# Optimization experiments

Measured on AMD Instinct MI355X. Metric: run time of the kernel, lower is better.

Reference implementation:

```python
import jax, jax.numpy as jnp
import numpy as np

N_EMBD = 1024
N_HEADS = 16
HEAD_DIM = N_EMBD // N_HEADS


def setup_inputs() -> dict:
    key = jax.random.key(0)
    ks = jax.random.split(key, 12)
    B, T, S, C = 2, 2048, 2048, N_EMBD
    std = 1.0 / np.sqrt(C)
    inp = {
        "x": jax.random.normal(ks[0], (B, T, C), dtype=jnp.float32),
        "context": jax.random.normal(ks[1], (B, S, C), dtype=jnp.float32),
        "q_w": jax.random.uniform(ks[2], (C, C), minval=-std, maxval=std, dtype=jnp.float32),
        "q_b": jax.random.uniform(ks[3], (C,), minval=-std, maxval=std, dtype=jnp.float32),
        "k_w": jax.random.uniform(ks[4], (C, C), minval=-std, maxval=std, dtype=jnp.float32),
        "k_b": jax.random.uniform(ks[5], (C,), minval=-std, maxval=std, dtype=jnp.float32),
        "v_w": jax.random.uniform(ks[6], (C, C), minval=-std, maxval=std, dtype=jnp.float32),
        "v_b": jax.random.uniform(ks[7], (C,), minval=-std, maxval=std, dtype=jnp.float32),
        "o_w": jax.random.uniform(ks[8], (C, C), minval=-std, maxval=std, dtype=jnp.float32),
        "o_b": jax.random.uniform(ks[9], (C,), minval=-std, maxval=std, dtype=jnp.float32),
    }
    return inp


def reference(x, context, q_w, q_b, k_w, k_b, v_w, v_b, o_w, o_b):
    B, T, C = x.shape
    S = context.shape[1]
    H, D = N_HEADS, HEAD_DIM
    # projections (torch Linear: y = x @ W^T + b; here weights stored as [in, out])
    q = (x @ q_w + q_b).reshape(B, T, H, D).transpose(0, 2, 1, 3)        # [B,H,T,D]
    k = (context @ k_w + k_b).reshape(B, S, H, D).transpose(0, 2, 1, 3)  # [B,H,S,D]
    v = (context @ v_w + v_b).reshape(B, S, H, D).transpose(0, 2, 1, 3)  # [B,H,S,D]
    att = jnp.einsum("bhtd,bhsd->bhts", q, k) / jnp.sqrt(jnp.float32(D))  # [B,H,T,S]
    causal = jnp.tril(jnp.ones((T, S), dtype=bool))                       # mask from tril buffer
    att = jnp.where(causal[None, None, :, :], att, -jnp.inf)
    att = jax.nn.softmax(att, axis=-1)
    y = jnp.einsum("bhts,bhsd->bhtd", att, v)                             # [B,H,T,D]
    y = y.transpose(0, 2, 1, 3).reshape(B, T, C)
    return y @ o_w + o_b
```

## Files before the change

kernel.cpp:

```cpp
#include <hip/hip_runtime.h>
#include <hip/hip_bf16.h>

using bf16 = __bf16;
using bf16x4 = __attribute__((ext_vector_type(4))) __bf16;
using bf16x8 = __attribute__((ext_vector_type(8))) __bf16;
using f32x4 = __attribute__((ext_vector_type(4))) float;
using u32 = unsigned int;

#define EXP2F(x) __builtin_amdgcn_exp2f(x)

__device__ __forceinline__ void gload16(const void* g, void* l) {
  __builtin_amdgcn_global_load_lds((const __attribute__((address_space(1))) u32*)g,
                                   (__attribute__((address_space(3))) u32*)l, 16, 0, 0);
}

__global__ __launch_bounds__(256) void cvt_kernel(const float4* __restrict__ a,
                                                  const float4* __restrict__ b,
                                                  bf16x4* __restrict__ out) {
  int g = blockIdx.x * blockDim.x + threadIdx.x;
  float4 v = (g < 1048576) ? a[g] : b[g - 1048576];
  bf16x4 o = {(bf16)v.x, (bf16)v.y, (bf16)v.z, (bf16)v.w};
  out[g] = o;
}

__global__ __launch_bounds__(256) void transpose_kernel(const float* __restrict__ w0,
                                                        const float* __restrict__ w1,
                                                        const float* __restrict__ w2,
                                                        const float* __restrict__ w3,
                                                        bf16* __restrict__ wtbase) {
  __shared__ float tile[32][33];
  const int z = blockIdx.z;
  const float* w = (z == 0) ? w0 : (z == 1) ? w1 : (z == 2) ? w2 : w3;
  bf16* wt = wtbase + (size_t)z * 1048576;
  int k0 = blockIdx.y * 32, n0 = blockIdx.x * 32;
  int tx = threadIdx.x, ty = threadIdx.y;
#pragma unroll
  for (int i = 0; i < 4; i++)
    tile[ty + i * 8][tx] = w[(size_t)(k0 + ty + i * 8) * 1024 + n0 + tx];
  __syncthreads();
#pragma unroll
  for (int i = 0; i < 4; i++)
    wt[(size_t)(n0 + ty + i * 8) * 1024 + k0 + tx] = (bf16)tile[tx][ty + i * 8];
}

template <int MODE>
__device__ __forceinline__ void gemm_body(char* __restrict__ smem,
                                          const bf16* __restrict__ A,
                                          const bf16* __restrict__ Bt,
                                          const float* __restrict__ bias,
                                          void* __restrict__ outp, int bx, int by,
                                          float oscale) {
  constexpr int K = 1024;
  bf16(*Cs)[136] = (bf16(*)[136])smem;

  const int tid = threadIdx.x;
  const int lane = tid & 63;
  const int w = tid >> 6;
  const int wr = w >> 1, wc = w & 1;
  const int m0 = by * 128, n0 = bx * 128;
  const int fr = lane & 15, lg = lane >> 4;

  const int p = lane & 3;
  const int r0 = w * 16 + (lane >> 2);
  const int r1 = r0 + 64;
  const char* gA0 = (const char*)(A + (size_t)(m0 + r0) * K) + ((p ^ ((r0 >> 1) & 3)) << 4);
  const char* gA1 = (const char*)(A + (size_t)(m0 + r1) * K) + ((p ^ ((r1 >> 1) & 3)) << 4);
  const char* gB0 = (const char*)(Bt + (size_t)(n0 + r0) * K) + ((p ^ ((r0 >> 1) & 3)) << 4);
  const char* gB1 = (const char*)(Bt + (size_t)(n0 + r1) * K) + ((p ^ ((r1 >> 1) & 3)) << 4);

  const int sA = (fr >> 1) & 3;
  int aoff[4], boff[4];
#pragma unroll
  for (int mi = 0; mi < 4; mi++)
    aoff[mi] = (wr * 64 + mi * 16 + fr) * 64 + ((lg ^ sA) << 4);
#pragma unroll
  for (int ni = 0; ni < 4; ni++)
    boff[ni] = 8192 + (wc * 64 + ni * 16 + fr) * 64 + ((lg ^ sA) << 4);

  f32x4 acc[4][4] = {};

  gload16(gA0, smem + w * 1024);
  gload16(gA1, smem + 4096 + w * 1024);
  gload16(gB0, smem + 8192 + w * 1024);
  gload16(gB1, smem + 12288 + w * 1024);

  int cur = 0;
  for (int k0 = 0; k0 < K; k0 += 32) {
    __syncthreads();
    if (k0 + 32 < K) {
      const int nb = (cur ^ 1) * 16384;
      const int go = (k0 + 32) * 2;
      gload16(gA0 + go, smem + nb + w * 1024);
      gload16(gA1 + go, smem + nb + 4096 + w * 1024);
      gload16(gB0 + go, smem + nb + 8192 + w * 1024);
      gload16(gB1 + go, smem + nb + 12288 + w * 1024);
    }
    const char* base = smem + cur * 16384;
    bf16x8 af[4], bfr[4];
#pragma unroll
    for (int mi = 0; mi < 4; mi++) af[mi] = *(const bf16x8*)(base + aoff[mi]);
#pragma unroll
    for (int ni = 0; ni < 4; ni++) bfr[ni] = *(const bf16x8*)(base + boff[ni]);
#pragma unroll
    for (int mi = 0; mi < 4; mi++)
#pragma unroll
      for (int ni = 0; ni < 4; ni++)
        acc[mi][ni] =
            __builtin_amdgcn_mfma_f32_16x16x32_bf16(af[mi], bfr[ni], acc[mi][ni], 0, 0, 0);
    cur ^= 1;
  }

  float bv[4];
#pragma unroll
  for (int ni = 0; ni < 4; ni++) bv[ni] = bias[n0 + wc * 64 + ni * 16 + fr];
#pragma unroll
  for (int mi = 0; mi < 4; mi++)
#pragma unroll
    for (int ni = 0; ni < 4; ni++)
#pragma unroll
      for (int j = 0; j < 4; j++) acc[mi][ni][j] = (acc[mi][ni][j] + bv[ni]) * oscale;

  if (MODE == 2) {
    float* O = (float*)outp;
#pragma unroll
    for (int mi = 0; mi < 4; mi++)
#pragma unroll
      for (int ni = 0; ni < 4; ni++)
#pragma unroll
        for (int j = 0; j < 4; j++) {
          int row = m0 + wr * 64 + mi * 16 + (lane >> 4) * 4 + j;
          int col = n0 + wc * 64 + ni * 16 + fr;
          O[(size_t)row * 1024 + col] = acc[mi][ni][j];
        }
    return;
  }

  __syncthreads();
#pragma unroll
  for (int mi = 0; mi < 4; mi++) {
    int r = wr * 64 + mi * 16 + (lane >> 4) * 4;
#pragma unroll
    for (int ni = 0; ni < 4; ni++) {
      int c = wc * 64 + ni * 16 + fr;
#pragma unroll
      for (int j = 0; j < 4; j++) Cs[r + j][c] = (bf16)acc[mi][ni][j];
    }
  }
  __syncthreads();

  bf16* O = (bf16*)outp;
  if (MODE == 0) {
    int row = tid >> 1, ch = (tid & 1) * 64;
    int rg = m0 + row;
    int b = rg >> 11, t_ = rg & 2047;
    int c0 = n0 + ch;
    int h = c0 >> 6;
    bf16* dst = O + ((size_t)(b * 16 + h) * 2048 + t_) * 64;
#pragma unroll
    for (int i = 0; i < 8; i++) *(bf16x8*)&dst[i * 8] = *(const bf16x8*)&Cs[row][ch + i * 8];
  } else {
    int colL = tid >> 1, sh = (tid & 1) * 64;
    int cg = n0 + colL;
    int h = cg >> 6, d = cg & 63;
    int rg = m0 + sh;
    int b = rg >> 11, s_ = rg & 2047;
    bf16* dst = O + ((size_t)((b * 16 + h) * 64 + d)) * 2048 + s_;
#pragma unroll
    for (int i = 0; i < 8; i++) {
      bf16x8 v;
#pragma unroll
      for (int jj = 0; jj < 8; jj++) v[jj] = Cs[sh + i * 8 + jj][colL];
      *(bf16x8*)&dst[i * 8] = v;
    }
  }
}

__global__ __launch_bounds__(256) void gemm_qkv_kernel(const bf16* __restrict__ xb,
                                                       const bf16* __restrict__ cb,
                                                       const bf16* __restrict__ wtbase,
                                                       const float* __restrict__ bq,
                                                       const float* __restrict__ bk,
                                                       const float* __restrict__ bv,
                                                       bf16* __restrict__ outbase) {
  __shared__ __align__(16) char smem[34816];
  const int lin = blockIdx.x;
  const int xcd = lin & 7, idx = lin >> 3;
  const int seq = xcd * 96 + idx;
  const int z = seq >> 8;
  const int rem = seq & 255;
  const int by = rem >> 3, bx = rem & 7;
  const bf16* A = (z == 0) ? xb : cb;
  const bf16* Wt = wtbase + (size_t)z * 1048576;
  const float* bias = (z == 0) ? bq : (z == 1) ? bk : bv;
  bf16* out = outbase + (size_t)z * 4194304;
  const float oscale = (z == 0) ? 0.125f * 1.4426950408889634f : 1.0f;
  if (z == 2)
    gemm_body<1>(smem, A, Wt, bias, (void*)out, bx, by, oscale);
  else
    gemm_body<0>(smem, A, Wt, bias, (void*)out, bx, by, oscale);
}

__global__ __launch_bounds__(256) void gemm_o_kernel(const bf16* __restrict__ A,
                                                     const bf16* __restrict__ Wt,
                                                     const float* __restrict__ bias,
                                                     float* __restrict__ out) {
  __shared__ __align__(16) char smem[34816];
  const int lin = blockIdx.x;
  const int xcd = lin & 7, idx = lin >> 3;
  const int seq = xcd * 32 + idx;
  const int by = seq >> 3, bx = seq & 7;
  gemm_body<2>(smem, A, Wt, bias, (void*)out, bx, by, 1.0f);
}

__global__ __launch_bounds__(256) void attn_kernel(const bf16* __restrict__ Q,
                                                   const bf16* __restrict__ Kc,
                                                   const bf16* __restrict__ Vt,
                                                   bf16* __restrict__ Y) {
  const int bh = blockIdx.x;
  const int qt = 31 - blockIdx.y;
  const int tid = threadIdx.x, lane = tid & 63, w = tid >> 6;
  const int lr = lane & 15, lg = lane >> 4;
  const int q0 = qt * 64 + w * 16;

  __shared__ __align__(16) bf16 Ks[64 * 64];
  __shared__ __align__(16) bf16 Vs[64 * 64];
  __shared__ __align__(16) bf16 Plds[4][16][72];

  const bf16* qb = Q + ((size_t)bh * 2048 + q0 + lr) * 64 + lg * 8;
  const bf16x8 qfB0 = *(const bf16x8*)qb;
  const bf16x8 qfB1 = *(const bf16x8*)(qb + 32);

  const bf16* Kbase = Kc + (size_t)bh * 2048 * 64;
  const bf16* Vbase = Vt + (size_t)bh * 64 * 2048;

  const int srow = tid >> 2;
  const int scol = (tid & 3) * 16;
  const int r7x = (srow & 7) * 8;
  const int d0 = srow * 64 + (scol ^ r7x);
  const int d1 = srow * 64 + ((scol + 8) ^ r7x);

  bf16x8 kr0, kr1, vr0, vr1;
  {
    const bf16* kp = Kbase + (size_t)srow * 64 + scol;
    kr0 = *(const bf16x8*)kp;
    kr1 = *(const bf16x8*)(kp + 8);
    const bf16* vp = Vbase + (size_t)srow * 2048 + scol;
    vr0 = *(const bf16x8*)vp;
    vr1 = *(const bf16x8*)(vp + 8);
  }

  f32x4 yacc[4] = {};
  float mrow = -__builtin_inff(), lrow = 0.0f;
  const int kxor = (lr & 7) * 8;

  for (int c = 0; c <= qt; ++c) {
    const int sbase = c * 64;
    __syncthreads();
    *(bf16x8*)&Ks[d0] = kr0;
    *(bf16x8*)&Ks[d1] = kr1;
    *(bf16x8*)&Vs[d0] = vr0;
    *(bf16x8*)&Vs[d1] = vr1;
    __syncthreads();

    {
      const int cn = (c < qt) ? c + 1 : c;
      const int sb = cn * 64;
      const bf16* kp = Kbase + (size_t)(sb + srow) * 64 + scol;
      kr0 = *(const bf16x8*)kp;
      kr1 = *(const bf16x8*)(kp + 8);
      const bf16* vp = Vbase + (size_t)srow * 2048 + sb + scol;
      vr0 = *(const bf16x8*)vp;
      vr1 = *(const bf16x8*)(vp + 8);
    }

    f32x4 st[4];
    __builtin_amdgcn_s_setprio(1);
#pragma unroll
    for (int h = 0; h < 4; ++h) {
      const int rb = (16 * h + lr) * 64;
      const bf16x8 kf0 = *(const bf16x8*)&Ks[rb + ((lg * 8) ^ kxor)];
      const bf16x8 kf1 = *(const bf16x8*)&Ks[rb + ((32 + lg * 8) ^ kxor)];
      f32x4 z = {};
      z = __builtin_amdgcn_mfma_f32_16x16x32_bf16(kf0, qfB0, z, 0, 0, 0);
      z = __builtin_amdgcn_mfma_f32_16x16x32_bf16(kf1, qfB1, z, 0, 0, 0);
      st[h] = z;
    }
    __builtin_amdgcn_s_setprio(0);
    if (c == qt) {
      const int qg = q0 + lr;
#pragma unroll
      for (int h = 0; h < 4; ++h)
#pragma unroll
        for (int j = 0; j < 4; ++j) {
          int sg = sbase + 16 * h + lg * 4 + j;
          if (sg > qg) st[h][j] = -__builtin_inff();
        }
    }
    float vmax = fmaxf(fmaxf(st[0][0], st[0][1]), fmaxf(st[0][2], st[0][3]));
#pragma unroll
    for (int h = 1; h < 4; ++h)
      vmax = fmaxf(vmax, fmaxf(fmaxf(st[h][0], st[h][1]), fmaxf(st[h][2], st[h][3])));
    vmax = fmaxf(vmax, __shfl_xor(vmax, 16));
    vmax = fmaxf(vmax, __shfl_xor(vmax, 32));

    if (!__all(vmax <= mrow)) {
      const float mnew = fmaxf(mrow, vmax);
      const float cf = EXP2F(mrow - mnew);
      mrow = mnew;
      lrow *= cf;
      float cfj[4];
#pragma unroll
      for (int j = 0; j < 4; ++j) cfj[j] = __shfl(cf, lg * 4 + j);
#pragma unroll
      for (int nf = 0; nf < 4; ++nf)
#pragma unroll
        for (int j = 0; j < 4; ++j) yacc[nf][j] *= cfj[j];
    }

    float rs = 0.0f;
#pragma unroll
    for (int h = 0; h < 4; ++h) {
      float p0 = EXP2F(st[h][0] - mrow);
      float p1 = EXP2F(st[h][1] - mrow);
      float p2 = EXP2F(st[h][2] - mrow);
      float p3 = EXP2F(st[h][3] - mrow);
      rs += (p0 + p1) + (p2 + p3);
      bf16x4 pk = {(bf16)p0, (bf16)p1, (bf16)p2, (bf16)p3};
      *(bf16x4*)&Plds[w][lr][16 * h + lg * 4] = pk;
    }
    rs += __shfl_xor(rs, 16);
    rs += __shfl_xor(rs, 32);
    lrow += rs;

    const bf16x8 pa0 = *(const bf16x8*)&Plds[w][lr][lg * 8];
    const bf16x8 pa1 = *(const bf16x8*)&Plds[w][lr][32 + lg * 8];
    __builtin_amdgcn_s_setprio(1);
#pragma unroll
    for (int nf = 0; nf < 4; ++nf) {
      const int rb = (nf * 16 + lr) * 64;
      const bf16x8 vf0 = *(const bf16x8*)&Vs[rb + ((lg * 8) ^ kxor)];
      const bf16x8 vf1 = *(const bf16x8*)&Vs[rb + ((32 + lg * 8) ^ kxor)];
      yacc[nf] = __builtin_amdgcn_mfma_f32_16x16x32_bf16(pa0, vf0, yacc[nf], 0, 0, 0);
      yacc[nf] = __builtin_amdgcn_mfma_f32_16x16x32_bf16(pa1, vf1, yacc[nf], 0, 0, 0);
    }
    __builtin_amdgcn_s_setprio(0);
  }

  const float rinv = 1.0f / lrow;
  float linv[4];
#pragma unroll
  for (int j = 0; j < 4; ++j) linv[j] = __shfl(rinv, lg * 4 + j);
  const int b = bh >> 4, h = bh & 15;
#pragma unroll
  for (int nf = 0; nf < 4; ++nf)
#pragma unroll
    for (int j = 0; j < 4; ++j) {
      int qg = q0 + lg * 4 + j;
      Y[((size_t)b * 2048 + qg) * 1024 + h * 64 + nf * 16 + lr] = (bf16)(yacc[nf][j] * linv[j]);
    }
}

extern "C" void kernel_launch(void* const* d_in, const int* in_sizes, int n_in,
                              void* d_out, int out_size, void* d_ws, size_t ws_size,
                              hipStream_t stream) {
  const float* x = (const float*)d_in[0];
  const float* ctx = (const float*)d_in[1];
  const float* q_w = (const float*)d_in[2];
  const float* q_b = (const float*)d_in[3];
  const float* k_w = (const float*)d_in[4];
  const float* k_b = (const float*)d_in[5];
  const float* v_w = (const float*)d_in[6];
  const float* v_b = (const float*)d_in[7];
  const float* o_w = (const float*)d_in[8];
  const float* o_b = (const float*)d_in[9];

  char* ws = (char*)d_ws;
  const size_t MB = 1024 * 1024;
  bf16* xb = (bf16*)(ws + 0);
  bf16* qwt = (bf16*)(ws + 16 * MB);
  bf16* Qws = (bf16*)(ws + 24 * MB);
  bf16* Kws = (bf16*)(ws + 32 * MB);
  bf16* Vt = (bf16*)(ws + 40 * MB);
  bf16* Yws = (bf16*)(ws + 48 * MB);
  bf16* owt = qwt + 3 * 1048576;
  bf16* cb = xb + 4194304;

  cvt_kernel<<<8192, 256, 0, stream>>>((const float4*)x, (const float4*)ctx, (bf16x4*)xb);

  dim3 tb(32, 8), tg(32, 32, 4);
  transpose_kernel<<<tg, tb, 0, stream>>>(q_w, k_w, v_w, o_w, qwt);

  gemm_qkv_kernel<<<768, 256, 0, stream>>>(xb, cb, qwt, q_b, k_b, v_b, Qws);

  attn_kernel<<<dim3(32, 32), 256, 0, stream>>>(Qws, Kws, Vt, Yws);

  gemm_o_kernel<<<256, 256, 0, stream>>>(Yws, owt, o_b, (float*)d_out);
}
```

Measured before the change: 117.8 us.

## Double attention query tile per wave and merge convert and transpose kernels

The attention kernel now gives each wave 32 query rows (two 16-row MFMA fragments) instead of 16, so every block covers 128 queries and each K/V chunk staged in LDS is reused across twice as many rows. The launch grid halves, and waves whose rows lie entirely before a chunk skip its compute to respect causality. Separately, the input bf16 conversion and the weight transpose are combined into one launch to save a kernel launch. In exchange, register pressure roughly doubles for the accumulators and softmax state, and causal load imbalance between waves in a block increases.

```diff
diff --git a/kernel.cpp b/kernel.cpp
--- a/kernel.cpp
+++ b/kernel.cpp
@@ -14,33 +14,37 @@
                                    (__attribute__((address_space(3))) u32*)l, 16, 0, 0);
 }
 
-__global__ __launch_bounds__(256) void cvt_kernel(const float4* __restrict__ a,
-                                                  const float4* __restrict__ b,
-                                                  bf16x4* __restrict__ out) {
-  int g = blockIdx.x * blockDim.x + threadIdx.x;
-  float4 v = (g < 1048576) ? a[g] : b[g - 1048576];
-  bf16x4 o = {(bf16)v.x, (bf16)v.y, (bf16)v.z, (bf16)v.w};
-  out[g] = o;
-}
-
-__global__ __launch_bounds__(256) void transpose_kernel(const float* __restrict__ w0,
-                                                        const float* __restrict__ w1,
-                                                        const float* __restrict__ w2,
-                                                        const float* __restrict__ w3,
-                                                        bf16* __restrict__ wtbase) {
+__global__ __launch_bounds__(256) void prep_kernel(const float4* __restrict__ x4,
+                                                   const float4* __restrict__ c4,
+                                                   bf16x4* __restrict__ xb4,
+                                                   const float* __restrict__ w0,
+                                                   const float* __restrict__ w1,
+                                                   const float* __restrict__ w2,
+                                                   const float* __restrict__ w3,
+                                                   bf16* __restrict__ wtbase) {
   __shared__ float tile[32][33];
-  const int z = blockIdx.z;
-  const float* w = (z == 0) ? w0 : (z == 1) ? w1 : (z == 2) ? w2 : w3;
-  bf16* wt = wtbase + (size_t)z * 1048576;
-  int k0 = blockIdx.y * 32, n0 = blockIdx.x * 32;
-  int tx = threadIdx.x, ty = threadIdx.y;
-#pragma unroll
-  for (int i = 0; i < 4; i++)
-    tile[ty + i * 8][tx] = w[(size_t)(k0 + ty + i * 8) * 1024 + n0 + tx];
-  __syncthreads();
-#pragma unroll
-  for (int i = 0; i < 4; i++)
-    wt[(size_t)(n0 + ty + i * 8) * 1024 + k0 + tx] = (bf16)tile[tx][ty + i * 8];
+  const int bid = blockIdx.x;
+  const int tid = threadIdx.x;
+  if (bid < 8192) {
+    int g = bid * 256 + tid;
+    float4 v = (g < 1048576) ? x4[g] : c4[g - 1048576];
+    bf16x4 o = {(bf16)v.x, (bf16)v.y, (bf16)v.z, (bf16)v.w};
+    xb4[g] = o;
+  } else {
+    const int t = bid - 8192;
+    const int z = t >> 10, rem = t & 1023;
+    const int n0 = (rem & 31) * 32, k0 = (rem >> 5) * 32;
+    const float* w = (z == 0) ? w0 : (z == 1) ? w1 : (z == 2) ? w2 : w3;
+    bf16* wt = wtbase + (size_t)z * 1048576;
+    const int tx = tid & 31, ty = tid >> 5;
+#pragma unroll
+    for (int i = 0; i < 4; i++)
+      tile[ty + i * 8][tx] = w[(size_t)(k0 + ty + i * 8) * 1024 + n0 + tx];
+    __syncthreads();
+#pragma unroll
+    for (int i = 0; i < 4; i++)
+      wt[(size_t)(n0 + ty + i * 8) * 1024 + k0 + tx] = (bf16)tile[tx][ty + i * 8];
+  }
 }
 
 template <int MODE>
@@ -217,18 +221,21 @@
                                                    const bf16* __restrict__ Vt,
                                                    bf16* __restrict__ Y) {
   const int bh = blockIdx.x;
-  const int qt = 31 - blockIdx.y;
+  const int tile = 15 - blockIdx.y;
+  const int q0t = tile * 128;
   const int tid = threadIdx.x, lane = tid & 63, w = tid >> 6;
   const int lr = lane & 15, lg = lane >> 4;
-  const int q0 = qt * 64 + w * 16;
+  const int qw = q0t + w * 32;
 
   __shared__ __align__(16) bf16 Ks[64 * 64];
   __shared__ __align__(16) bf16 Vs[64 * 64];
-  __shared__ __align__(16) bf16 Plds[4][16][72];
-
-  const bf16* qb = Q + ((size_t)bh * 2048 + q0 + lr) * 64 + lg * 8;
-  const bf16x8 qfB0 = *(const bf16x8*)qb;
-  const bf16x8 qfB1 = *(const bf16x8*)(qb + 32);
+  __shared__ __align__(16) bf16 Plds[4][32][72];
+
+  const bf16* qb = Q + ((size_t)bh * 2048 + qw + lr) * 64 + lg * 8;
+  const bf16x8 qf00 = *(const bf16x8*)qb;
+  const bf16x8 qf01 = *(const bf16x8*)(qb + 32);
+  const bf16x8 qf10 = *(const bf16x8*)(qb + 1024);
+  const bf16x8 qf11 = *(const bf16x8*)(qb + 1056);
 
   const bf16* Kbase = Kc + (size_t)bh * 2048 * 64;
   const bf16* Vbase = Vt + (size_t)bh * 64 * 2048;
@@ -249,11 +256,13 @@
     vr1 = *(const bf16x8*)(vp + 8);
   }
 
-  f32x4 yacc[4] = {};
-  float mrow = -__builtin_inff(), lrow = 0.0f;
+  f32x4 yacc0[4] = {}, yacc1[4] = {};
+  float mrow0 = -__builtin_inff(), mrow1 = -__builtin_inff();
+  float lrow0 = 0.0f, lrow1 = 0.0f;
   const int kxor = (lr & 7) * 8;
-
-  for (int c = 0; c <= qt; ++c) {
+  const int nchunk = 2 * tile + 2;
+
+  for (int c = 0; c < nchunk; ++c) {
     const int sbase = c * 64;
     __syncthreads();
     *(bf16x8*)&Ks[d0] = kr0;
@@ -263,7 +272,7 @@
     __syncthreads();
 
     {
-      const int cn = (c < qt) ? c + 1 : c;
+      const int cn = (c + 1 < nchunk) ? c + 1 : c;
       const int sb = cn * 64;
       const bf16* kp = Kbase + (size_t)(sb + srow) * 64 + scol;
       kr0 = *(const bf16x8*)kp;
@@ -273,90 +282,131 @@
       vr1 = *(const bf16x8*)(vp + 8);
     }
 
-    f32x4 st[4];
+    if (sbase > qw + 31) continue;
+
+    f32x4 st0[4], st1[4];
     __builtin_amdgcn_s_setprio(1);
 #pragma unroll
     for (int h = 0; h < 4; ++h) {
       const int rb = (16 * h + lr) * 64;
       const bf16x8 kf0 = *(const bf16x8*)&Ks[rb + ((lg * 8) ^ kxor)];
       const bf16x8 kf1 = *(const bf16x8*)&Ks[rb + ((32 + lg * 8) ^ kxor)];
-      f32x4 z = {};
-      z = __builtin_amdgcn_mfma_f32_16x16x32_bf16(kf0, qfB0, z, 0, 0, 0);
-      z = __builtin_amdgcn_mfma_f32_16x16x32_bf16(kf1, qfB1, z, 0, 0, 0);
-      st[h] = z;
+      f32x4 z0 = {}, z1 = {};
+      z0 = __builtin_amdgcn_mfma_f32_16x16x32_bf16(kf0, qf00, z0, 0, 0, 0);
+      z0 = __builtin_amdgcn_mfma_f32_16x16x32_bf16(kf1, qf01, z0, 0, 0, 0);
+      z1 = __builtin_amdgcn_mfma_f32_16x16x32_bf16(kf0, qf10, z1, 0, 0, 0);
+      z1 = __builtin_amdgcn_mfma_f32_16x16x32_bf16(kf1, qf11, z1, 0, 0, 0);
+      st0[h] = z0;
+      st1[h] = z1;
     }
     __builtin_amdgcn_s_setprio(0);
-    if (c == qt) {
-      const int qg = q0 + lr;
+
+    if (sbase + 63 > qw) {
+      const int qg0 = qw + lr, qg1 = qw + 16 + lr;
 #pragma unroll
       for (int h = 0; h < 4; ++h)
 #pragma unroll
         for (int j = 0; j < 4; ++j) {
           int sg = sbase + 16 * h + lg * 4 + j;
-          if (sg > qg) st[h][j] = -__builtin_inff();
+          if (sg > qg0) st0[h][j] = -__builtin_inff();
+          if (sg > qg1) st1[h][j] = -__builtin_inff();
         }
     }
-    float vmax = fmaxf(fmaxf(st[0][0], st[0][1]), fmaxf(st[0][2], st[0][3]));
-#pragma unroll
-    for (int h = 1; h < 4; ++h)
-      vmax = fmaxf(vmax, fmaxf(fmaxf(st[h][0], st[h][1]), fmaxf(st[h][2], st[h][3])));
-    vmax = fmaxf(vmax, __shfl_xor(vmax, 16));
-    vmax = fmaxf(vmax, __shfl_xor(vmax, 32));
-
-    if (!__all(vmax <= mrow)) {
-      const float mnew = fmaxf(mrow, vmax);
-      const float cf = EXP2F(mrow - mnew);
-      mrow = mnew;
-      lrow *= cf;
+
+    float vmax0 = fmaxf(fmaxf(st0[0][0], st0[0][1]), fmaxf(st0[0][2], st0[0][3]));
+    float vmax1 = fmaxf(fmaxf(st1[0][0], st1[0][1]), fmaxf(st1[0][2], st1[0][3]));
+#pragma unroll
+    for (int h = 1; h < 4; ++h) {
+      vmax0 = fmaxf(vmax0, fmaxf(fmaxf(st0[h][0], st0[h][1]), fmaxf(st0[h][2], st0[h][3])));
+      vmax1 = fmaxf(vmax1, fmaxf(fmaxf(st1[h][0], st1[h][1]), fmaxf(st1[h][2], st1[h][3])));
+    }
+    vmax0 = fmaxf(vmax0, __shfl_xor(vmax0, 16));
+    vmax0 = fmaxf(vmax0, __shfl_xor(vmax0, 32));
+    vmax1 = fmaxf(vmax1, __shfl_xor(vmax1, 16));
+    vmax1 = fmaxf(vmax1, __shfl_xor(vmax1, 32));
+
+    if (!__all(vmax0 <= mrow0)) {
+      const float mnew = fmaxf(mrow0, vmax0);
+      const float cf = EXP2F(mrow0 - mnew);
+      mrow0 = mnew;
+      lrow0 *= cf;
       float cfj[4];
 #pragma unroll
       for (int j = 0; j < 4; ++j) cfj[j] = __shfl(cf, lg * 4 + j);
 #pragma unroll
       for (int nf = 0; nf < 4; ++nf)
 #pragma unroll
-        for (int j = 0; j < 4; ++j) yacc[nf][j] *= cfj[j];
-    }
-
-    float rs = 0.0f;
+        for (int j = 0; j < 4; ++j) yacc0[nf][j] *= cfj[j];
+    }
+    if (!__all(vmax1 <= mrow1)) {
+      const float mnew = fmaxf(mrow1, vmax1);
+      const float cf = EXP2F(mrow1 - mnew);
+      mrow1 = mnew;
+      lrow1 *= cf;
+      float cfj[4];
+#pragma unroll
+      for (int j = 0; j < 4; ++j) cfj[j] = __shfl(cf, lg * 4 + j);
+#pragma unroll
+      for (int nf = 0; nf < 4; ++nf)
+#pragma unroll
+        for (int j = 0; j < 4; ++j) yacc1[nf][j] *= cfj[j];
+    }
+
+    float rs0 = 0.0f, rs1 = 0.0f;
 #pragma unroll
     for (int h = 0; h < 4; ++h) {
-      float p0 = EXP2F(st[h][0] - mrow);
-      float p1 = EXP2F(st[h][1] - mrow);
-      float p2 = EXP2F(st[h][2] - mrow);
-      float p3 = EXP2F(st[h][3] - mrow);
-      rs += (p0 + p1) + (p2 + p3);
-      bf16x4 pk = {(bf16)p0, (bf16)p1, (bf16)p2, (bf16)p3};
-      *(bf16x4*)&Plds[w][lr][16 * h + lg * 4] = pk;
-    }
-    rs += __shfl_xor(rs, 16);
-    rs += __shfl_xor(rs, 32);
-    lrow += rs;
-
-    const bf16x8 pa0 = *(const bf16x8*)&Plds[w][lr][lg * 8];
-    const bf16x8 pa1 = *(const bf16x8*)&Plds[w][lr][32 + lg * 8];
+      float a0 = EXP2F(st0[h][0] - mrow0), a1 = EXP2F(st0[h][1] - mrow0);
+      float a2 = EXP2F(st0[h][2] - mrow0), a3 = EXP2F(st0[h][3] - mrow0);
+      rs0 += (a0 + a1) + (a2 + a3);
+      bf16x4 pk0 = {(bf16)a0, (bf16)a1, (bf16)a2, (bf16)a3};
+      *(bf16x4*)&Plds[w][lr][16 * h + lg * 4] = pk0;
+      float b0 = EXP2F(st1[h][0] - mrow1), b1 = EXP2F(st1[h][1] - mrow1);
+      float b2 = EXP2F(st1[h][2] - mrow1), b3 = EXP2F(st1[h][3] - mrow1);
+      rs1 += (b0 + b1) + (b2 + b3);
+      bf16x4 pk1 = {(bf16)b0, (bf16)b1, (bf16)b2, (bf16)b3};
+      *(bf16x4*)&Plds[w][16 + lr][16 * h + lg * 4] = pk1;
+    }
+    rs0 += __shfl_xor(rs0, 16);
+    rs0 += __shfl_xor(rs0, 32);
+    rs1 += __shfl_xor(rs1, 16);
+    rs1 += __shfl_xor(rs1, 32);
+    lrow0 += rs0;
+    lrow1 += rs1;
+
+    const bf16x8 pa00 = *(const bf16x8*)&Plds[w][lr][lg * 8];
+    const bf16x8 pa01 = *(const bf16x8*)&Plds[w][lr][32 + lg * 8];
+    const bf16x8 pa10 = *(const bf16x8*)&Plds[w][16 + lr][lg * 8];
+    const bf16x8 pa11 = *(const bf16x8*)&Plds[w][16 + lr][32 + lg * 8];
     __builtin_amdgcn_s_setprio(1);
 #pragma unroll
     for (int nf = 0; nf < 4; ++nf) {
       const int rb = (nf * 16 + lr) * 64;
       const bf16x8 vf0 = *(const bf16x8*)&Vs[rb + ((lg * 8) ^ kxor)];
       const bf16x8 vf1 = *(const bf16x8*)&Vs[rb + ((32 + lg * 8) ^ kxor)];
-      yacc[nf] = __builtin_amdgcn_mfma_f32_16x16x32_bf16(pa0, vf0, yacc[nf], 0, 0, 0);
-      yacc[nf] = __builtin_amdgcn_mfma_f32_16x16x32_bf16(pa1, vf1, yacc[nf], 0, 0, 0);
+      yacc0[nf] = __builtin_amdgcn_mfma_f32_16x16x32_bf16(pa00, vf0, yacc0[nf], 0, 0, 0);
+      yacc0[nf] = __builtin_amdgcn_mfma_f32_16x16x32_bf16(pa01, vf1, yacc0[nf], 0, 0, 0);
+      yacc1[nf] = __builtin_amdgcn_mfma_f32_16x16x32_bf16(pa10, vf0, yacc1[nf], 0, 0, 0);
+      yacc1[nf] = __builtin_amdgcn_mfma_f32_16x16x32_bf16(pa11, vf1, yacc1[nf], 0, 0, 0);
     }
     __builtin_amdgcn_s_setprio(0);
   }
 
-  const float rinv = 1.0f / lrow;
-  float linv[4];
-#pragma unroll
-  for (int j = 0; j < 4; ++j) linv[j] = __shfl(rinv, lg * 4 + j);
+  const float rinv0 = 1.0f / lrow0, rinv1 = 1.0f / lrow1;
+  float linv0[4], linv1[4];
+#pragma unroll
+  for (int j = 0; j < 4; ++j) {
+    linv0[j] = __shfl(rinv0, lg * 4 + j);
+    linv1[j] = __shfl(rinv1, lg * 4 + j);
+  }
   const int b = bh >> 4, h = bh & 15;
 #pragma unroll
   for (int nf = 0; nf < 4; ++nf)
 #pragma unroll
     for (int j = 0; j < 4; ++j) {
-      int qg = q0 + lg * 4 + j;
-      Y[((size_t)b * 2048 + qg) * 1024 + h * 64 + nf * 16 + lr] = (bf16)(yacc[nf][j] * linv[j]);
+      int qg0 = qw + lg * 4 + j;
+      Y[((size_t)b * 2048 + qg0) * 1024 + h * 64 + nf * 16 + lr] = (bf16)(yacc0[nf][j] * linv0[j]);
+      int qg1 = qg0 + 16;
+      Y[((size_t)b * 2048 + qg1) * 1024 + h * 64 + nf * 16 + lr] = (bf16)(yacc1[nf][j] * linv1[j]);
     }
 }
 
@@ -385,14 +435,12 @@
   bf16* owt = qwt + 3 * 1048576;
   bf16* cb = xb + 4194304;
 
-  cvt_kernel<<<8192, 256, 0, stream>>>((const float4*)x, (const float4*)ctx, (bf16x4*)xb);
-
-  dim3 tb(32, 8), tg(32, 32, 4);
-  transpose_kernel<<<tg, tb, 0, stream>>>(q_w, k_w, v_w, o_w, qwt);
+  prep_kernel<<<12288, 256, 0, stream>>>((const float4*)x, (const float4*)ctx, (bf16x4*)xb,
+                                         q_w, k_w, v_w, o_w, qwt);
 
   gemm_qkv_kernel<<<768, 256, 0, stream>>>(xb, cb, qwt, q_b, k_b, v_b, Qws);
 
-  attn_kernel<<<dim3(32, 32), 256, 0, stream>>>(Qws, Kws, Vt, Yws);
+  attn_kernel<<<dim3(32, 16), 256, 0, stream>>>(Qws, Kws, Vt, Yws);
 
   gemm_o_kernel<<<256, 256, 0, stream>>>(Yws, owt, o_b, (float*)d_out);
 }
```

After: 130.2 us. 1.11x slower.

## Triple-buffer GEMM K-loop with vmcnt waits and merge prep kernels

Applied to the files above, without the earlier changes.

The GEMM main loop goes from a double-buffered LDS pipeline with a full barrier per step to a three-stage ring buffer. Loads are issued two tiles ahead, and an explicit s_waitcnt vmcnt(4) plus a raw s_barrier lets one tile's loads stay in flight during compute. Shared memory grows to 48KB, which may reduce occupancy. Separately, the fp32-to-bf16 conversion and weight-transpose kernels are fused into one launch to save a kernel launch.

```diff
diff --git a/kernel.cpp b/kernel.cpp
--- a/kernel.cpp
+++ b/kernel.cpp
@@ -14,33 +14,37 @@
                                    (__attribute__((address_space(3))) u32*)l, 16, 0, 0);
 }
 
-__global__ __launch_bounds__(256) void cvt_kernel(const float4* __restrict__ a,
-                                                  const float4* __restrict__ b,
-                                                  bf16x4* __restrict__ out) {
-  int g = blockIdx.x * blockDim.x + threadIdx.x;
-  float4 v = (g < 1048576) ? a[g] : b[g - 1048576];
-  bf16x4 o = {(bf16)v.x, (bf16)v.y, (bf16)v.z, (bf16)v.w};
-  out[g] = o;
-}
-
-__global__ __launch_bounds__(256) void transpose_kernel(const float* __restrict__ w0,
-                                                        const float* __restrict__ w1,
-                                                        const float* __restrict__ w2,
-                                                        const float* __restrict__ w3,
-                                                        bf16* __restrict__ wtbase) {
+__global__ __launch_bounds__(256) void prep_kernel(const float4* __restrict__ x4,
+                                                   const float4* __restrict__ c4,
+                                                   bf16x4* __restrict__ xb4,
+                                                   const float* __restrict__ w0,
+                                                   const float* __restrict__ w1,
+                                                   const float* __restrict__ w2,
+                                                   const float* __restrict__ w3,
+                                                   bf16* __restrict__ wtbase) {
   __shared__ float tile[32][33];
-  const int z = blockIdx.z;
-  const float* w = (z == 0) ? w0 : (z == 1) ? w1 : (z == 2) ? w2 : w3;
-  bf16* wt = wtbase + (size_t)z * 1048576;
-  int k0 = blockIdx.y * 32, n0 = blockIdx.x * 32;
-  int tx = threadIdx.x, ty = threadIdx.y;
-#pragma unroll
-  for (int i = 0; i < 4; i++)
-    tile[ty + i * 8][tx] = w[(size_t)(k0 + ty + i * 8) * 1024 + n0 + tx];
-  __syncthreads();
-#pragma unroll
-  for (int i = 0; i < 4; i++)
-    wt[(size_t)(n0 + ty + i * 8) * 1024 + k0 + tx] = (bf16)tile[tx][ty + i * 8];
+  const int bid = blockIdx.x;
+  const int tid = threadIdx.x;
+  if (bid < 8192) {
+    int g = bid * 256 + tid;
+    float4 v = (g < 1048576) ? x4[g] : c4[g - 1048576];
+    bf16x4 o = {(bf16)v.x, (bf16)v.y, (bf16)v.z, (bf16)v.w};
+    xb4[g] = o;
+  } else {
+    const int t = bid - 8192;
+    const int z = t >> 10, rem = t & 1023;
+    const int n0 = (rem & 31) * 32, k0 = (rem >> 5) * 32;
+    const float* w = (z == 0) ? w0 : (z == 1) ? w1 : (z == 2) ? w2 : w3;
+    bf16* wt = wtbase + (size_t)z * 1048576;
+    const int tx = tid & 31, ty = tid >> 5;
+#pragma unroll
+    for (int i = 0; i < 4; i++)
+      tile[ty + i * 8][tx] = w[(size_t)(k0 + ty + i * 8) * 1024 + n0 + tx];
+    __syncthreads();
+#pragma unroll
+    for (int i = 0; i < 4; i++)
+      wt[(size_t)(n0 + ty + i * 8) * 1024 + k0 + tx] = (bf16)tile[tx][ty + i * 8];
+  }
 }
 
 template <int MODE>
@@ -79,23 +83,32 @@
 
   f32x4 acc[4][4] = {};
 
-  gload16(gA0, smem + w * 1024);
-  gload16(gA1, smem + 4096 + w * 1024);
-  gload16(gB0, smem + 8192 + w * 1024);
-  gload16(gB1, smem + 12288 + w * 1024);
-
-  int cur = 0;
-  for (int k0 = 0; k0 < K; k0 += 32) {
-    __syncthreads();
-    if (k0 + 32 < K) {
-      const int nb = (cur ^ 1) * 16384;
-      const int go = (k0 + 32) * 2;
-      gload16(gA0 + go, smem + nb + w * 1024);
-      gload16(gA1 + go, smem + nb + 4096 + w * 1024);
-      gload16(gB0 + go, smem + nb + 8192 + w * 1024);
-      gload16(gB1 + go, smem + nb + 12288 + w * 1024);
-    }
-    const char* base = smem + cur * 16384;
+  auto stage = [&](int t, int buf) {
+    char* b = smem + buf * 16384;
+    const int go = t * 64;
+    gload16(gA0 + go, b + w * 1024);
+    gload16(gA1 + go, b + 4096 + w * 1024);
+    gload16(gB0 + go, b + 8192 + w * 1024);
+    gload16(gB1 + go, b + 12288 + w * 1024);
+  };
+
+  stage(0, 0);
+  stage(1, 1);
+
+  int cb = 0;
+  for (int it = 0; it < 32; ++it) {
+    if (it < 31)
+      asm volatile("s_waitcnt vmcnt(4)" ::: "memory");
+    else
+      asm volatile("s_waitcnt vmcnt(0)" ::: "memory");
+    __builtin_amdgcn_s_barrier();
+    __builtin_amdgcn_sched_barrier(0);
+    if (it + 2 < 32) {
+      int nb = cb - 1;
+      if (nb < 0) nb = 2;
+      stage(it + 2, nb);
+    }
+    const char* base = smem + cb * 16384;
     bf16x8 af[4], bfr[4];
 #pragma unroll
     for (int mi = 0; mi < 4; mi++) af[mi] = *(const bf16x8*)(base + aoff[mi]);
@@ -107,9 +120,10 @@
       for (int ni = 0; ni < 4; ni++)
         acc[mi][ni] =
             __builtin_amdgcn_mfma_f32_16x16x32_bf16(af[mi], bfr[ni], acc[mi][ni], 0, 0, 0);
-    cur ^= 1;
-  }
-
+    cb = (cb == 2) ? 0 : cb + 1;
+  }
+
+  asm volatile("" ::: "memory");
   float bv[4];
 #pragma unroll
   for (int ni = 0; ni < 4; ni++) bv[ni] = bias[n0 + wc * 64 + ni * 16 + fr];
@@ -182,7 +196,7 @@
                                                        const float* __restrict__ bk,
                                                        const float* __restrict__ bv,
                                                        bf16* __restrict__ outbase) {
-  __shared__ __align__(16) char smem[34816];
+  __shared__ __align__(16) char smem[49152];
   const int lin = blockIdx.x;
   const int xcd = lin & 7, idx = lin >> 3;
   const int seq = xcd * 96 + idx;
@@ -204,7 +218,7 @@
                                                      const bf16* __restrict__ Wt,
                                                      const float* __restrict__ bias,
                                                      float* __restrict__ out) {
-  __shared__ __align__(16) char smem[34816];
+  __shared__ __align__(16) char smem[49152];
   const int lin = blockIdx.x;
   const int xcd = lin & 7, idx = lin >> 3;
   const int seq = xcd * 32 + idx;
@@ -385,10 +399,8 @@
   bf16* owt = qwt + 3 * 1048576;
   bf16* cb = xb + 4194304;
 
-  cvt_kernel<<<8192, 256, 0, stream>>>((const float4*)x, (const float4*)ctx, (bf16x4*)xb);
-
-  dim3 tb(32, 8), tg(32, 32, 4);
-  transpose_kernel<<<tg, tb, 0, stream>>>(q_w, k_w, v_w, o_w, qwt);
+  prep_kernel<<<12288, 256, 0, stream>>>((const float4*)x, (const float4*)ctx, (bf16x4*)xb,
+                                         q_w, k_w, v_w, o_w, qwt);
 
   gemm_qkv_kernel<<<768, 256, 0, stream>>>(xb, cb, qwt, q_b, k_b, v_b, Qws);
 
```

Result: faster. 111.5 us (-5.4%).
